# Performance work log

Hardware: AMD Instinct MI355X
Metric: run time of the kernel (lower is better)

Reference implementation:

```python
import jax, jax.numpy as jnp
import numpy as np

PN, KN, MBON, DAN = 3, 50, 10, 10
DT = 0.5
TAU = 1.0          # kenyon/apl/mbon/dan tau
RC = 5.0           # kenyon & dan lowpass RC
TAU_W = 2.0        # mbon tau_weights


def setup_inputs() -> dict:
    key = jax.random.key(0)
    ks = jax.random.split(key, 16)
    T, B = 128, 32768
    n = lambda k, shape, s=0.5: jax.random.normal(k, shape, dtype=jnp.float32) * s
    return {
        "odor": jax.random.normal(ks[0], (T, B, PN), dtype=jnp.float32),
        "context": jax.random.uniform(ks[1], (T, B, 1), dtype=jnp.float32),
        # KenyonCell
        "pn_weight": n(ks[2], (B, PN, KN)),
        "kn_bias": n(ks[3], (KN,)),
        # APLCell
        "apl_kc_weight": jnp.ones((KN, 1), dtype=jnp.float32),
        "apl_bias": jnp.full((1,), -0.5, dtype=jnp.float32),
        # MBONCell
        "mbon_dan_weight": n(ks[4], (DAN, MBON)),
        "mbon_bias": n(ks[5], (MBON,)),
        # DANCell
        "dan_mbon_weight": n(ks[6], (MBON, DAN)),
        "dan_dan_weight": n(ks[7], (DAN, DAN)),
        "dan_context_weight": n(ks[8], (1, DAN)),
        "dan_bias": n(ks[9], (DAN,)),
        # decoder Linear(10, 2)
        "dec_W": n(ks[10], (2, MBON), 0.3),
        "dec_b": n(ks[11], (2,), 0.1),
        # plastic KC->MBON weights and their activation trace
        "kc_weight0": n(ks[12], (B, KN, MBON)),
        "wact0": jnp.zeros((B, KN, MBON), dtype=jnp.float32),
    }


def _run(odor, context, pn_weight, kn_bias, apl_kc_weight, apl_bias,
         mbon_dan_weight, mbon_bias, dan_mbon_weight, dan_dan_weight,
         dan_context_weight, dan_bias, dec_W, dec_b, kc_weight0, wact0):
    B = odor.shape[1]
    dt_tau = DT / TAU
    alpha = DT / (DT + RC)          # lowpass coefficient (same RC for KC and DAN)
    dt_tauw = DT / TAU_W
    relu = jax.nn.relu

    def step(carry, xs):
        kc, apl, mbon, dan, low_kc, low_dan, kc_w, wact = carry
        odor_t, ctx_t = xs            # [B,PN], [B,1]
        # KenyonCell: per-batch PN->KC matmul, APL inhibition (ones weight -> broadcast)
        pn_value = jnp.einsum('bp,bpk->bk', odor_t, pn_weight)      # [B,KN]
        kc_n = kc * (1 - dt_tau) + dt_tau * relu(pn_value - apl + kn_bias)
        # APLCell
        apl_n = apl * (1 - dt_tau) + dt_tau * relu(kc_n @ apl_kc_weight + apl_bias)
        # MBONCell: plastic per-batch KC->MBON weights, DAN gating
        kc_value = jnp.einsum('bk,bkm->bm', kc_n, kc_w)             # [B,MBON]
        dan_mod = jax.nn.sigmoid(dan @ mbon_dan_weight)             # [B,MBON]
        mbon_n = mbon * (1 - dt_tau) + dt_tau * dan_mod * relu(kc_value + mbon_bias)
        # DANCell
        dan_pre = dan @ dan_dan_weight + mbon_n @ dan_mbon_weight + ctx_t @ dan_context_weight + dan_bias
        dan_n = dan * (1 - dt_tau) + dt_tau * relu(dan_pre)
        # low-pass traces
        low_kc_n = alpha * kc_n + (1 - alpha) * low_kc
        low_dan_n = alpha * dan_n + (1 - alpha) * low_dan
        # plasticity: weights blend toward OLD activation trace, trace integrates new activity
        syn = kc_n[:, :, None] * low_dan_n[:, None, :] - low_kc[:, :, None] * dan_n[:, None, :]
        # note: torch code uses state_low_kc AFTER update -> low_kc_n; keep faithful:
        syn = kc_n[:, :, None] * low_dan_n[:, None, :] - low_kc_n[:, :, None] * dan_n[:, None, :]
        wact_n = wact + DT * syn
        kc_w_n = kc_w * (1 - dt_tauw) + dt_tauw * wact
        out = mbon_n @ dec_W.T + dec_b                              # [B,2]
        return (kc_n, apl_n, mbon_n, dan_n, low_kc_n, low_dan_n, kc_w_n, wact_n), out

    z = lambda *s: jnp.zeros(s, dtype=jnp.float32)
    carry0 = (z(B, KN), z(B, 1), z(B, MBON), z(B, DAN), z(B, KN), z(B, DAN), kc_weight0, wact0)
    _, outs = jax.lax.scan(step, carry0, (odor, context))
    return outs                                                     # [T,B,2]


def reference(odor, context, pn_weight, kn_bias, apl_kc_weight, apl_bias,
              mbon_dan_weight, mbon_bias, dan_mbon_weight, dan_dan_weight,
              dan_context_weight, dan_bias, dec_W, dec_b, kc_weight0, wact0):
    return _run(odor, context, pn_weight, kn_bias, apl_kc_weight, apl_bias,
                mbon_dan_weight, mbon_bias, dan_mbon_weight, dan_dan_weight,
                dan_context_weight, dan_bias, dec_W, dec_b, kc_weight0, wact0)
```

## Files before the change

### kernel.cpp

```cpp
#include <hip/hip_runtime.h>

#define KN  50
#define NM  10
#define LPB 16

typedef float v2f __attribute__((ext_vector_type(2)));

template <int CTRL>
__device__ __forceinline__ float dpp_add(float x) {
  return x + __int_as_float(
      __builtin_amdgcn_update_dpp(0, __float_as_int(x), CTRL, 0xF, 0xF, true));
}

__device__ __forceinline__ float rowsum16(float x) {
  x = dpp_add<0x121>(x);
  x = dpp_add<0x122>(x);
  x = dpp_add<0x124>(x);
  x = dpp_add<0x128>(x);
  return x;
}

__device__ __forceinline__ float bcast(int idx4, float x) {
  return __int_as_float(__builtin_amdgcn_ds_bpermute(idx4, __float_as_int(x)));
}

extern "C" __global__ void __launch_bounds__(256)
__attribute__((amdgpu_waves_per_eu(2, 2)))
fly_kernel(const float* __restrict__ odor,
           const float* __restrict__ ctxp,
           const float* __restrict__ pn_w,
           const float* __restrict__ kn_b,
           const float* __restrict__ apl_w,
           const float* __restrict__ apl_b,
           const float* __restrict__ mdw_g,
           const float* __restrict__ mbon_b,
           const float* __restrict__ dmw_g,
           const float* __restrict__ ddw_g,
           const float* __restrict__ dcw_g,
           const float* __restrict__ dan_b,
           const float* __restrict__ decW,
           const float* __restrict__ decb,
           const float* __restrict__ kcw0,
           const float* __restrict__ wact0,
           float* __restrict__ out,
           int B, int T)
{
  const int tid   = threadIdx.x;
  const int j     = tid & (LPB - 1);
  const int jhalf = j >> 1;
  const int jodd  = j & 1;
  const int b     = blockIdx.x * (256 / LPB) + (tid >> 4);
  if (b >= B) return;

  const int base4 = (tid & 48) << 2;
  const bool has4 = (j + 48) < KN;

  v2f   kcw[4][5], wct[4][5];
  float pw0[4], pw1[4], pw2[4], knb[4], aw[4];
  float kcn[4] = {0.f,0.f,0.f,0.f}, lkc[4] = {0.f,0.f,0.f,0.f};

  #pragma unroll
  for (int i = 0; i < 4; ++i) {
    const int k = j + 16 * i;
    if (i < 3 || has4) {
      const v2f* a = reinterpret_cast<const v2f*>(kcw0  + ((size_t)b * KN + k) * NM);
      const v2f* w = reinterpret_cast<const v2f*>(wact0 + ((size_t)b * KN + k) * NM);
      #pragma unroll
      for (int h = 0; h < 5; ++h) { kcw[i][h] = a[h]; wct[i][h] = w[h]; }
      pw0[i] = pn_w[((size_t)b * 3 + 0) * KN + k];
      pw1[i] = pn_w[((size_t)b * 3 + 1) * KN + k];
      pw2[i] = pn_w[((size_t)b * 3 + 2) * KN + k];
      knb[i] = kn_b[k];
      aw[i]  = apl_w[k];
    } else {
      #pragma unroll
      for (int h = 0; h < 5; ++h) { kcw[i][h] = (v2f)(0.f); wct[i][h] = (v2f)(0.f); }
      pw0[i] = pw1[i] = pw2[i] = 0.f; knb[i] = 0.f; aw[i] = 0.f;
    }
  }

  v2f   mdw2[5], ddw2[5];
  float dmw[NM];
  float cw = 0.f, db_ = 0.f, mb_ = 0.f, dw0 = 0.f, dw1 = 0.f;
  #pragma unroll
  for (int h = 0; h < 5; ++h) { mdw2[h] = (v2f)(0.f); ddw2[h] = (v2f)(0.f); }
  #pragma unroll
  for (int m = 0; m < NM; ++m) dmw[m] = 0.f;
  if (j < NM) {
    #pragma unroll
    for (int h = 0; h < 5; ++h) {
      mdw2[h].x = mdw_g[(2*h)   * NM + j];  mdw2[h].y = mdw_g[(2*h+1) * NM + j];
      ddw2[h].x = ddw_g[(2*h)   * NM + j];  ddw2[h].y = ddw_g[(2*h+1) * NM + j];
    }
    #pragma unroll
    for (int m = 0; m < NM; ++m) dmw[m] = dmw_g[m * NM + j];
    cw  = dcw_g[j];
    db_ = dan_b[j];
    mb_ = mbon_b[j];
    dw0 = decW[j];
    dw1 = decW[NM + j];
  }
  const float aplb = apl_b[0];
  const float db0 = decb[0], db1 = decb[1];

  const float ALPHA = (float)(0.5 / 5.5);

  float apl = 0.f, mbon_m = 0.f, dan_m = 0.f;
  v2f dvec2[5], ldv2[5];
  #pragma unroll
  for (int h = 0; h < 5; ++h) { dvec2[h] = (v2f)(0.f); ldv2[h] = (v2f)(0.f); }

  size_t ob = (size_t)b * 3;
  float o0n = odor[ob], o1n = odor[ob + 1], o2n = odor[ob + 2];
  float cxn = ctxp[b];

  for (int t = 0; t < T; ++t) {
    const float o0 = o0n, o1 = o1n, o2 = o2n, cx = cxn;
    {
      const int tn = (t + 1 < T) ? t + 1 : t;
      const size_t obn = ((size_t)tn * B + b) * 3;
      o0n = odor[obn]; o1n = odor[obn + 1]; o2n = odor[obn + 2];
      cxn = ctxp[(size_t)tn * B + b];
    }

    float psum = 0.f;
    v2f p2[5];
    #pragma unroll
    for (int h = 0; h < 5; ++h) p2[h] = (v2f)(0.f);

    #pragma unroll
    for (int i = 0; i < 4; ++i) {
      if (i < 3 || has4) {
        float pv = fmaf(pw0[i], o0, fmaf(pw1[i], o1, pw2[i] * o2));
        float r  = fmaxf(pv - apl + knb[i], 0.f);
        float kn = 0.5f * (kcn[i] + r);
        kcn[i] = kn;
        lkc[i] = fmaf(ALPHA, kn - lkc[i], lkc[i]);
        psum = fmaf(kn, aw[i], psum);
        #pragma unroll
        for (int h = 0; h < 5; ++h) p2[h] += kn * kcw[i][h];
      }
    }

    psum = rowsum16(psum);
    #pragma unroll
    for (int h = 0; h < 5; ++h) {
      p2[h].x = rowsum16(p2[h].x);
      p2[h].y = rowsum16(p2[h].y);
    }

    apl = 0.5f * apl + 0.5f * fmaxf(psum + aplb, 0.f);

    v2f rsel = p2[0];
    #pragma unroll
    for (int h = 1; h < 5; ++h) rsel = (jhalf == h) ? p2[h] : rsel;
    const float kcv = jodd ? rsel.y : rsel.x;

    v2f s2 = dvec2[0] * mdw2[0];
    #pragma unroll
    for (int e = 1; e < 5; ++e) s2 += dvec2[e] * mdw2[e];
    const float s = s2.x + s2.y;
    const float dmod = 1.f / (1.f + __expf(-s));
    mbon_m = 0.5f * mbon_m + 0.5f * dmod * fmaxf(kcv + mb_, 0.f);

    v2f dp2 = dvec2[0] * ddw2[0];
    #pragma unroll
    for (int e = 1; e < 5; ++e) dp2 += dvec2[e] * ddw2[e];
    float dp = dp2.x + dp2.y + fmaf(cx, cw, db_);
    #pragma unroll
    for (int m = 0; m < NM; ++m)
      dp = fmaf(bcast(base4 + 4 * m, mbon_m), dmw[m], dp);
    dan_m = 0.5f * dan_m + 0.5f * fmaxf(dp, 0.f);

    #pragma unroll
    for (int e = 0; e < 5; ++e) {
      dvec2[e].x = bcast(base4 + 8 * e,     dan_m);
      dvec2[e].y = bcast(base4 + 8 * e + 4, dan_m);
      ldv2[e] += ALPHA * (dvec2[e] - ldv2[e]);
    }

    const float q0 = rowsum16(mbon_m * dw0) + db0;
    const float q1 = rowsum16(mbon_m * dw1) + db1;
    if (j == 0) {
      float2 st; st.x = q0; st.y = q1;
      *reinterpret_cast<float2*>(out + ((size_t)t * B + b) * 2) = st;
    }

    #pragma unroll
    for (int i = 0; i < 4; ++i) {
      if (i < 3 || has4) {
        const float kh  =  0.5f * kcn[i];
        const float nlh = -0.5f * lkc[i];
        #pragma unroll
        for (int h = 0; h < 5; ++h) {
          const v2f w = wct[i][h];
          kcw[i][h] = 0.75f * kcw[i][h] + 0.25f * w;
          wct[i][h] = w + kh * ldv2[h] + nlh * dvec2[h];
        }
      }
    }
  }
}

extern "C" void kernel_launch(void* const* d_in, const int* in_sizes, int n_in,
                              void* d_out, int out_size, void* d_ws, size_t ws_size,
                              hipStream_t stream) {
  const float* odor   = (const float*)d_in[0];
  const float* ctx    = (const float*)d_in[1];
  const float* pn_w   = (const float*)d_in[2];
  const float* kn_b   = (const float*)d_in[3];
  const float* apl_w  = (const float*)d_in[4];
  const float* apl_b  = (const float*)d_in[5];
  const float* mdw    = (const float*)d_in[6];
  const float* mbon_b = (const float*)d_in[7];
  const float* dmw    = (const float*)d_in[8];
  const float* ddw    = (const float*)d_in[9];
  const float* dcw    = (const float*)d_in[10];
  const float* dan_b  = (const float*)d_in[11];
  const float* decW   = (const float*)d_in[12];
  const float* decb   = (const float*)d_in[13];
  const float* kcw0   = (const float*)d_in[14];
  const float* wact0  = (const float*)d_in[15];
  float* out = (float*)d_out;

  const int B = in_sizes[14] / (KN * NM);
  const int T = in_sizes[0] / (B * 3);

  const int batches_per_block = 256 / LPB;
  dim3 grid((B + batches_per_block - 1) / batches_per_block);
  dim3 block(256);
  hipLaunchKernelGGL(fly_kernel, grid, block, 0, stream,
                     odor, ctx, pn_w, kn_b, apl_w, apl_b,
                     mdw, mbon_b, dmw, ddw, dcw, dan_b,
                     decW, decb, kcw0, wact0, out, B, T);
}
```

Before: 824.2 us.

## Move wact trace to per-thread LDS slots and pack KC math into float2

Moves the per-thread 40-float plastic activation trace (wact) out of registers into a padded per-thread LDS region, lowering VGPR pressure. The waves_per_eu(2,2) cap is removed so occupancy can rise. The KC update is rewritten as packed float2 ops, and the odor/context prefetch is replaced by direct pointer-stepped loads. The trade is extra LDS reads and writes every step, about 43 KB of LDS per block that may itself limit occupancy, and odor loads that are no longer prefetched a step ahead.

```diff
diff --git a/kernel.cpp b/kernel.cpp
--- a/kernel.cpp
+++ b/kernel.cpp
@@ -3,6 +3,7 @@
 #define KN  50
 #define NM  10
 #define LPB 16
+#define WSTRIDE 42
 
 typedef float v2f __attribute__((ext_vector_type(2)));
 
@@ -25,7 +26,6 @@
 }
 
 extern "C" __global__ void __launch_bounds__(256)
-__attribute__((amdgpu_waves_per_eu(2, 2)))
 fly_kernel(const float* __restrict__ odor,
            const float* __restrict__ ctxp,
            const float* __restrict__ pn_w,
@@ -45,6 +45,8 @@
            float* __restrict__ out,
            int B, int T)
 {
+  __shared__ float smem[256 * WSTRIDE];
+
   const int tid   = threadIdx.x;
   const int j     = tid & (LPB - 1);
   const int jhalf = j >> 1;
@@ -53,37 +55,53 @@
   if (b >= B) return;
 
   const int base4 = (tid & 48) << 2;
-  const bool has4 = (j + 48) < KN;
-
-  v2f   kcw[4][5], wct[4][5];
-  float pw0[4], pw1[4], pw2[4], knb[4], aw[4];
-  float kcn[4] = {0.f,0.f,0.f,0.f}, lkc[4] = {0.f,0.f,0.f,0.f};
-
+  v2f* __restrict__ wlds = reinterpret_cast<v2f*>(&smem[tid * WSTRIDE]);
+
+  v2f kcw[4][5];
   #pragma unroll
   for (int i = 0; i < 4; ++i) {
     const int k = j + 16 * i;
-    if (i < 3 || has4) {
+    if (k < KN) {
       const v2f* a = reinterpret_cast<const v2f*>(kcw0  + ((size_t)b * KN + k) * NM);
       const v2f* w = reinterpret_cast<const v2f*>(wact0 + ((size_t)b * KN + k) * NM);
       #pragma unroll
-      for (int h = 0; h < 5; ++h) { kcw[i][h] = a[h]; wct[i][h] = w[h]; }
-      pw0[i] = pn_w[((size_t)b * 3 + 0) * KN + k];
-      pw1[i] = pn_w[((size_t)b * 3 + 1) * KN + k];
-      pw2[i] = pn_w[((size_t)b * 3 + 2) * KN + k];
-      knb[i] = kn_b[k];
-      aw[i]  = apl_w[k];
+      for (int h = 0; h < 5; ++h) { kcw[i][h] = a[h]; wlds[i * 5 + h] = w[h]; }
     } else {
-      #pragma unroll
-      for (int h = 0; h < 5; ++h) { kcw[i][h] = (v2f)(0.f); wct[i][h] = (v2f)(0.f); }
-      pw0[i] = pw1[i] = pw2[i] = 0.f; knb[i] = 0.f; aw[i] = 0.f;
-    }
+      v2f zz; zz.x = 0.f; zz.y = 0.f;
+      #pragma unroll
+      for (int h = 0; h < 5; ++h) { kcw[i][h] = zz; wlds[i * 5 + h] = zz; }
+    }
+  }
+
+  v2f pw0v[2], pw1v[2], pw2v[2], knbv[2], awv[2], kcnv[2], lkcv[2];
+  #pragma unroll
+  for (int q = 0; q < 2; ++q) {
+    float c0[2], c1[2], c2[2], cb[2], ca[2];
+    #pragma unroll
+    for (int h2 = 0; h2 < 2; ++h2) {
+      const int k = j + 16 * (2 * q + h2);
+      if (k < KN) {
+        c0[h2] = pn_w[((size_t)b * 3 + 0) * KN + k];
+        c1[h2] = pn_w[((size_t)b * 3 + 1) * KN + k];
+        c2[h2] = pn_w[((size_t)b * 3 + 2) * KN + k];
+        cb[h2] = kn_b[k];
+        ca[h2] = apl_w[k];
+      } else { c0[h2]=c1[h2]=c2[h2]=cb[h2]=ca[h2]=0.f; }
+    }
+    pw0v[q].x = c0[0]; pw0v[q].y = c0[1];
+    pw1v[q].x = c1[0]; pw1v[q].y = c1[1];
+    pw2v[q].x = c2[0]; pw2v[q].y = c2[1];
+    knbv[q].x = cb[0]; knbv[q].y = cb[1];
+    awv[q].x  = ca[0]; awv[q].y  = ca[1];
+    kcnv[q].x = 0.f; kcnv[q].y = 0.f;
+    lkcv[q].x = 0.f; lkcv[q].y = 0.f;
   }
 
   v2f   mdw2[5], ddw2[5];
   float dmw[NM];
   float cw = 0.f, db_ = 0.f, mb_ = 0.f, dw0 = 0.f, dw1 = 0.f;
   #pragma unroll
-  for (int h = 0; h < 5; ++h) { mdw2[h] = (v2f)(0.f); ddw2[h] = (v2f)(0.f); }
+  for (int h = 0; h < 5; ++h) { mdw2[h].x = 0.f; mdw2[h].y = 0.f; ddw2[h].x = 0.f; ddw2[h].y = 0.f; }
   #pragma unroll
   for (int m = 0; m < NM; ++m) dmw[m] = 0.f;
   if (j < NM) {
@@ -102,47 +120,47 @@
   }
   const float aplb = apl_b[0];
   const float db0 = decb[0], db1 = decb[1];
-
   const float ALPHA = (float)(0.5 / 5.5);
 
   float apl = 0.f, mbon_m = 0.f, dan_m = 0.f;
   v2f dvec2[5], ldv2[5];
   #pragma unroll
-  for (int h = 0; h < 5; ++h) { dvec2[h] = (v2f)(0.f); ldv2[h] = (v2f)(0.f); }
-
-  size_t ob = (size_t)b * 3;
-  float o0n = odor[ob], o1n = odor[ob + 1], o2n = odor[ob + 2];
-  float cxn = ctxp[b];
+  for (int h = 0; h < 5; ++h) { dvec2[h].x = 0.f; dvec2[h].y = 0.f; ldv2[h].x = 0.f; ldv2[h].y = 0.f; }
+
+  const float* op = odor + (size_t)b * 3;
+  const float* cp = ctxp + b;
+  float* outp = out + (size_t)b * 2;
+  const size_t B3 = (size_t)B * 3;
 
   for (int t = 0; t < T; ++t) {
-    const float o0 = o0n, o1 = o1n, o2 = o2n, cx = cxn;
-    {
-      const int tn = (t + 1 < T) ? t + 1 : t;
-      const size_t obn = ((size_t)tn * B + b) * 3;
-      o0n = odor[obn]; o1n = odor[obn + 1]; o2n = odor[obn + 2];
-      cxn = ctxp[(size_t)tn * B + b];
-    }
-
-    float psum = 0.f;
+    const float o0 = op[0], o1 = op[1], o2 = op[2];  op += B3;
+    const float cx = *cp;                            cp += B;
+
+    float kns[4], lks[4];
+    v2f psum2; psum2.x = 0.f; psum2.y = 0.f;
     v2f p2[5];
     #pragma unroll
-    for (int h = 0; h < 5; ++h) p2[h] = (v2f)(0.f);
-
+    for (int h = 0; h < 5; ++h) { p2[h].x = 0.f; p2[h].y = 0.f; }
+
+    #pragma unroll
+    for (int q = 0; q < 2; ++q) {
+      v2f pv  = pw0v[q] * o0 + pw1v[q] * o1 + pw2v[q] * o2;
+      v2f arg = pv + knbv[q] - apl;
+      v2f r; r.x = fmaxf(arg.x, 0.f); r.y = fmaxf(arg.y, 0.f);
+      v2f kn = 0.5f * (kcnv[q] + r);
+      kcnv[q] = kn;
+      lkcv[q] = lkcv[q] + ALPHA * (kn - lkcv[q]);
+      psum2 += kn * awv[q];
+      kns[2*q] = kn.x;      kns[2*q+1] = kn.y;
+      lks[2*q] = lkcv[q].x; lks[2*q+1] = lkcv[q].y;
+    }
     #pragma unroll
     for (int i = 0; i < 4; ++i) {
-      if (i < 3 || has4) {
-        float pv = fmaf(pw0[i], o0, fmaf(pw1[i], o1, pw2[i] * o2));
-        float r  = fmaxf(pv - apl + knb[i], 0.f);
-        float kn = 0.5f * (kcn[i] + r);
-        kcn[i] = kn;
-        lkc[i] = fmaf(ALPHA, kn - lkc[i], lkc[i]);
-        psum = fmaf(kn, aw[i], psum);
-        #pragma unroll
-        for (int h = 0; h < 5; ++h) p2[h] += kn * kcw[i][h];
-      }
-    }
-
-    psum = rowsum16(psum);
+      #pragma unroll
+      for (int h = 0; h < 5; ++h) p2[h] += kns[i] * kcw[i][h];
+    }
+
+    const float psum = rowsum16(psum2.x + psum2.y);
     #pragma unroll
     for (int h = 0; h < 5; ++h) {
       p2[h].x = rowsum16(p2[h].x);
@@ -183,20 +201,21 @@
     const float q1 = rowsum16(mbon_m * dw1) + db1;
     if (j == 0) {
       float2 st; st.x = q0; st.y = q1;
-      *reinterpret_cast<float2*>(out + ((size_t)t * B + b) * 2) = st;
-    }
+      *reinterpret_cast<float2*>(outp) = st;
+    }
+    outp += (size_t)B * 2;
 
     #pragma unroll
     for (int i = 0; i < 4; ++i) {
-      if (i < 3 || has4) {
-        const float kh  =  0.5f * kcn[i];
-        const float nlh = -0.5f * lkc[i];
-        #pragma unroll
-        for (int h = 0; h < 5; ++h) {
-          const v2f w = wct[i][h];
-          kcw[i][h] = 0.75f * kcw[i][h] + 0.25f * w;
-          wct[i][h] = w + kh * ldv2[h] + nlh * dvec2[h];
-        }
+      const float kh  =  0.5f * kns[i];
+      const float nlh = -0.5f * lks[i];
+      v2f w[5];
+      #pragma unroll
+      for (int h = 0; h < 5; ++h) w[h] = wlds[i * 5 + h];
+      #pragma unroll
+      for (int h = 0; h < 5; ++h) {
+        kcw[i][h] = 0.75f * kcw[i][h] + 0.25f * w[h];
+        wlds[i * 5 + h] = w[h] + kh * ldv2[h] + nlh * dvec2[h];
       }
     }
   }
```

Result: slower. 1.133 ms (+37.5%).

## Spread each batch over 32 lanes instead of 16 with two KC rows per lane

Applied to the files above, without the earlier changes.

Each batch element now uses 32 lanes, so a lane holds two Kenyon-cell rows of the plastic weights instead of four. Reductions go to a 32-wide sum built from DPP row sums plus a ds_swizzle. The KC state and PN weights are packed into two-wide vectors, and the MBON-to-DAN broadcast is vectorised. The waves-per-EU cap is dropped, which halves per-lane register state and should raise occupancy, at the cost of twice the threads, an extra swizzle per reduction, and more lanes idling in the 10-wide MBON/DAN stages.

```diff
diff --git a/kernel.cpp b/kernel.cpp
--- a/kernel.cpp
+++ b/kernel.cpp
@@ -2,7 +2,7 @@
 
 #define KN  50
 #define NM  10
-#define LPB 16
+#define LPB 32
 
 typedef float v2f __attribute__((ext_vector_type(2)));
 
@@ -20,12 +20,16 @@
   return x;
 }
 
+__device__ __forceinline__ float rowsum32(float x) {
+  x = rowsum16(x);
+  return x + __int_as_float(__builtin_amdgcn_ds_swizzle(__float_as_int(x), 0x401F));
+}
+
 __device__ __forceinline__ float bcast(int idx4, float x) {
   return __int_as_float(__builtin_amdgcn_ds_bpermute(idx4, __float_as_int(x)));
 }
 
 extern "C" __global__ void __launch_bounds__(256)
-__attribute__((amdgpu_waves_per_eu(2, 2)))
 fly_kernel(const float* __restrict__ odor,
            const float* __restrict__ ctxp,
            const float* __restrict__ pn_w,
@@ -49,51 +53,61 @@
   const int j     = tid & (LPB - 1);
   const int jhalf = j >> 1;
   const int jodd  = j & 1;
-  const int b     = blockIdx.x * (256 / LPB) + (tid >> 4);
+  const int b     = blockIdx.x * (256 / LPB) + (tid >> 5);
   if (b >= B) return;
 
-  const int base4 = (tid & 48) << 2;
-  const bool has4 = (j + 48) < KN;
-
-  v2f   kcw[4][5], wct[4][5];
-  float pw0[4], pw1[4], pw2[4], knb[4], aw[4];
-  float kcn[4] = {0.f,0.f,0.f,0.f}, lkc[4] = {0.f,0.f,0.f,0.f};
-
-  #pragma unroll
-  for (int i = 0; i < 4; ++i) {
-    const int k = j + 16 * i;
-    if (i < 3 || has4) {
-      const v2f* a = reinterpret_cast<const v2f*>(kcw0  + ((size_t)b * KN + k) * NM);
-      const v2f* w = reinterpret_cast<const v2f*>(wact0 + ((size_t)b * KN + k) * NM);
+  const int base4 = (tid & 32) << 2;
+  const int k2    = j + 32;
+  const bool has2 = k2 < KN;
+
+  v2f kcw[2][5], wct[2][5];
+  {
+    const v2f* a0 = reinterpret_cast<const v2f*>(kcw0  + ((size_t)b * KN + j) * NM);
+    const v2f* w0 = reinterpret_cast<const v2f*>(wact0 + ((size_t)b * KN + j) * NM);
+    #pragma unroll
+    for (int h = 0; h < 5; ++h) { kcw[0][h] = a0[h]; wct[0][h] = w0[h]; }
+    if (has2) {
+      const v2f* a1 = reinterpret_cast<const v2f*>(kcw0  + ((size_t)b * KN + k2) * NM);
+      const v2f* w1 = reinterpret_cast<const v2f*>(wact0 + ((size_t)b * KN + k2) * NM);
       #pragma unroll
-      for (int h = 0; h < 5; ++h) { kcw[i][h] = a[h]; wct[i][h] = w[h]; }
-      pw0[i] = pn_w[((size_t)b * 3 + 0) * KN + k];
-      pw1[i] = pn_w[((size_t)b * 3 + 1) * KN + k];
-      pw2[i] = pn_w[((size_t)b * 3 + 2) * KN + k];
-      knb[i] = kn_b[k];
-      aw[i]  = apl_w[k];
+      for (int h = 0; h < 5; ++h) { kcw[1][h] = a1[h]; wct[1][h] = w1[h]; }
     } else {
+      v2f zz; zz.x = 0.f; zz.y = 0.f;
       #pragma unroll
-      for (int h = 0; h < 5; ++h) { kcw[i][h] = (v2f)(0.f); wct[i][h] = (v2f)(0.f); }
-      pw0[i] = pw1[i] = pw2[i] = 0.f; knb[i] = 0.f; aw[i] = 0.f;
-    }
-  }
-
-  v2f   mdw2[5], ddw2[5];
-  float dmw[NM];
+      for (int h = 0; h < 5; ++h) { kcw[1][h] = zz; wct[1][h] = zz; }
+    }
+  }
+
+  v2f pw0, pw1, pw2, knb, aw, kcn, lkc;
+  pw0.x = pn_w[((size_t)b * 3 + 0) * KN + j];
+  pw1.x = pn_w[((size_t)b * 3 + 1) * KN + j];
+  pw2.x = pn_w[((size_t)b * 3 + 2) * KN + j];
+  knb.x = kn_b[j];
+  aw.x  = apl_w[j];
+  if (has2) {
+    pw0.y = pn_w[((size_t)b * 3 + 0) * KN + k2];
+    pw1.y = pn_w[((size_t)b * 3 + 1) * KN + k2];
+    pw2.y = pn_w[((size_t)b * 3 + 2) * KN + k2];
+    knb.y = kn_b[k2];
+    aw.y  = apl_w[k2];
+  } else { pw0.y = 0.f; pw1.y = 0.f; pw2.y = 0.f; knb.y = 0.f; aw.y = 0.f; }
+  kcn.x = 0.f; kcn.y = 0.f; lkc.x = 0.f; lkc.y = 0.f;
+
+  v2f mdw2[5], ddw2[5], dmw2[5];
   float cw = 0.f, db_ = 0.f, mb_ = 0.f, dw0 = 0.f, dw1 = 0.f;
   #pragma unroll
-  for (int h = 0; h < 5; ++h) { mdw2[h] = (v2f)(0.f); ddw2[h] = (v2f)(0.f); }
-  #pragma unroll
-  for (int m = 0; m < NM; ++m) dmw[m] = 0.f;
+  for (int h = 0; h < 5; ++h) {
+    mdw2[h].x = 0.f; mdw2[h].y = 0.f;
+    ddw2[h].x = 0.f; ddw2[h].y = 0.f;
+    dmw2[h].x = 0.f; dmw2[h].y = 0.f;
+  }
   if (j < NM) {
     #pragma unroll
     for (int h = 0; h < 5; ++h) {
       mdw2[h].x = mdw_g[(2*h)   * NM + j];  mdw2[h].y = mdw_g[(2*h+1) * NM + j];
       ddw2[h].x = ddw_g[(2*h)   * NM + j];  ddw2[h].y = ddw_g[(2*h+1) * NM + j];
-    }
-    #pragma unroll
-    for (int m = 0; m < NM; ++m) dmw[m] = dmw_g[m * NM + j];
+      dmw2[h].x = dmw_g[(2*h)   * NM + j];  dmw2[h].y = dmw_g[(2*h+1) * NM + j];
+    }
     cw  = dcw_g[j];
     db_ = dan_b[j];
     mb_ = mbon_b[j];
@@ -102,51 +116,44 @@
   }
   const float aplb = apl_b[0];
   const float db0 = decb[0], db1 = decb[1];
-
   const float ALPHA = (float)(0.5 / 5.5);
 
   float apl = 0.f, mbon_m = 0.f, dan_m = 0.f;
   v2f dvec2[5], ldv2[5];
   #pragma unroll
-  for (int h = 0; h < 5; ++h) { dvec2[h] = (v2f)(0.f); ldv2[h] = (v2f)(0.f); }
-
-  size_t ob = (size_t)b * 3;
-  float o0n = odor[ob], o1n = odor[ob + 1], o2n = odor[ob + 2];
-  float cxn = ctxp[b];
+  for (int h = 0; h < 5; ++h) { dvec2[h].x = 0.f; dvec2[h].y = 0.f; ldv2[h].x = 0.f; ldv2[h].y = 0.f; }
+
+  const float* op = odor + (size_t)b * 3;
+  const float* cp = ctxp + b;
+  float* outp = out + (size_t)b * 2;
+  const size_t B3 = (size_t)B * 3;
+
+  float o0 = op[0], o1 = op[1], o2 = op[2];
+  float cx = *cp;
 
   for (int t = 0; t < T; ++t) {
-    const float o0 = o0n, o1 = o1n, o2 = o2n, cx = cxn;
-    {
-      const int tn = (t + 1 < T) ? t + 1 : t;
-      const size_t obn = ((size_t)tn * B + b) * 3;
-      o0n = odor[obn]; o1n = odor[obn + 1]; o2n = odor[obn + 2];
-      cxn = ctxp[(size_t)tn * B + b];
-    }
-
-    float psum = 0.f;
+    const float* opn = (t + 1 < T) ? op + B3 : op;
+    const float* cpn = (t + 1 < T) ? cp + B  : cp;
+    const float o0n = opn[0], o1n = opn[1], o2n = opn[2];
+    const float cxn = *cpn;
+
+    v2f pv  = pw0 * o0 + pw1 * o1 + pw2 * o2;
+    v2f arg = pv + knb - apl;
+    v2f r; r.x = fmaxf(arg.x, 0.f); r.y = fmaxf(arg.y, 0.f);
+    v2f kn = 0.5f * (kcn + r);
+    kcn = kn;
+    lkc = lkc + ALPHA * (kn - lkc);
+    v2f psum2 = kn * aw;
+
     v2f p2[5];
     #pragma unroll
-    for (int h = 0; h < 5; ++h) p2[h] = (v2f)(0.f);
-
-    #pragma unroll
-    for (int i = 0; i < 4; ++i) {
-      if (i < 3 || has4) {
-        float pv = fmaf(pw0[i], o0, fmaf(pw1[i], o1, pw2[i] * o2));
-        float r  = fmaxf(pv - apl + knb[i], 0.f);
-        float kn = 0.5f * (kcn[i] + r);
-        kcn[i] = kn;
-        lkc[i] = fmaf(ALPHA, kn - lkc[i], lkc[i]);
-        psum = fmaf(kn, aw[i], psum);
-        #pragma unroll
-        for (int h = 0; h < 5; ++h) p2[h] += kn * kcw[i][h];
-      }
-    }
-
-    psum = rowsum16(psum);
+    for (int h = 0; h < 5; ++h) p2[h] = kn.x * kcw[0][h] + kn.y * kcw[1][h];
+
+    const float psum = rowsum32(psum2.x + psum2.y);
     #pragma unroll
     for (int h = 0; h < 5; ++h) {
-      p2[h].x = rowsum16(p2[h].x);
-      p2[h].y = rowsum16(p2[h].y);
+      p2[h].x = rowsum32(p2[h].x);
+      p2[h].y = rowsum32(p2[h].y);
     }
 
     apl = 0.5f * apl + 0.5f * fmaxf(psum + aplb, 0.f);
@@ -166,10 +173,14 @@
     v2f dp2 = dvec2[0] * ddw2[0];
     #pragma unroll
     for (int e = 1; e < 5; ++e) dp2 += dvec2[e] * ddw2[e];
-    float dp = dp2.x + dp2.y + fmaf(cx, cw, db_);
-    #pragma unroll
-    for (int m = 0; m < NM; ++m)
-      dp = fmaf(bcast(base4 + 4 * m, mbon_m), dmw[m], dp);
+    #pragma unroll
+    for (int e = 0; e < 5; ++e) {
+      v2f mv;
+      mv.x = bcast(base4 + 8 * e,     mbon_m);
+      mv.y = bcast(base4 + 8 * e + 4, mbon_m);
+      dp2 += mv * dmw2[e];
+    }
+    const float dp = dp2.x + dp2.y + fmaf(cx, cw, db_);
     dan_m = 0.5f * dan_m + 0.5f * fmaxf(dp, 0.f);
 
     #pragma unroll
@@ -183,22 +194,25 @@
     const float q1 = rowsum16(mbon_m * dw1) + db1;
     if (j == 0) {
       float2 st; st.x = q0; st.y = q1;
-      *reinterpret_cast<float2*>(out + ((size_t)t * B + b) * 2) = st;
-    }
-
-    #pragma unroll
-    for (int i = 0; i < 4; ++i) {
-      if (i < 3 || has4) {
-        const float kh  =  0.5f * kcn[i];
-        const float nlh = -0.5f * lkc[i];
-        #pragma unroll
-        for (int h = 0; h < 5; ++h) {
-          const v2f w = wct[i][h];
-          kcw[i][h] = 0.75f * kcw[i][h] + 0.25f * w;
-          wct[i][h] = w + kh * ldv2[h] + nlh * dvec2[h];
-        }
+      *reinterpret_cast<float2*>(outp) = st;
+    }
+    outp += (size_t)B * 2;
+
+    {
+      const float kh0  =  0.5f * kcn.x, kh1  =  0.5f * kcn.y;
+      const float nlh0 = -0.5f * lkc.x, nlh1 = -0.5f * lkc.y;
+      #pragma unroll
+      for (int h = 0; h < 5; ++h) {
+        const v2f w0 = wct[0][h], w1 = wct[1][h];
+        kcw[0][h] = 0.75f * kcw[0][h] + 0.25f * w0;
+        kcw[1][h] = 0.75f * kcw[1][h] + 0.25f * w1;
+        wct[0][h] = w0 + kh0 * ldv2[h] + nlh0 * dvec2[h];
+        wct[1][h] = w1 + kh1 * ldv2[h] + nlh1 * dvec2[h];
       }
     }
+
+    o0 = o0n; o1 = o1n; o2 = o2n; cx = cxn;
+    op = opn; cp = cpn;
   }
 }
 
```

Result: slower. 1.166 ms (+41.5%).
